# Optimization experiments

Hardware: AMD Instinct MI355X
Metric: run time of the kernel (lower is better)

Reference implementation:

```python
import jax, jax.numpy as jnp
import numpy as np

B = 2097152


def _pairwise_overlap(amin, amax, bmin, bmax):
    # amin/amax: [B,4]; bmin/bmax: [B,4] -> pairwise overlap [B,4,4]
    lo = jnp.maximum(amin[:, :, None], bmin[:, None, :])
    hi = jnptofloat = jnp.minimum(amax[:, :, None], bmax[:, None, :])
    return jnp.maximum(0.0, hi - lo)


def _self_beta(xmin, xmax, ymin, ymax):
    # sum over 4x4 pairs; diagonal terms squared, off-diagonal plain.
    xo = _pairwise_overlap(xmin, xmax, xmin, xmax)  # [B,4,4]
    yo = _pairwise_overlap(ymin, ymax, ymin, ymax)  # [B,4,4]
    area = xo * yo
    eye = jnp.eye(4, dtype=bool)
    return jnp.sum(jnp.where(eye, area * area, area), axis=(1, 2))  # [B]


def setup_inputs() -> dict:
    key = jax.random.key(0)
    k1, k2 = jax.random.split(key)
    true = jax.random.uniform(k1, (B, 4, 4), dtype=jnp.float32)
    pred = jax.random.uniform(k2, (B, 10, 3), dtype=jnp.float32)
    return {"true": true, "pred": pred}


def reference(true, pred):
    # true: [B,4,4] -> per-box coords, each [B,4]
    minx1, miny1, maxx1, maxy1 = [true[:, :, i] for i in range(4)]
    # pred: [B,10,3] -> columns [B,10]; only first 4 boxes used by the 4x4 loops
    fminx, miny2, fmaxx = pred[:, :, 0], pred[:, :, 1], pred[:, :, 2]
    minx2 = jnp.minimum(fminx, fmaxx)
    maxx2 = jnp.maximum(fminx, fmaxx)
    maxy2 = miny2 + (maxx2 - minx2)
    minx2, maxx2, miny2, maxy2 = (a[:, :4] for a in (minx2, maxx2, miny2, maxy2))

    # intersection: sum over all 4x4 (true_i, pred_j) pairs
    xo = _pairwise_overlap(minx1, maxx1, minx2, maxx2)
    yo = _pairwise_overlap(miny1, maxy1, miny2, maxy2)
    intersection = jnp.sum(xo * yo, axis=(1, 2))  # [B]

    beta1 = _self_beta(minx1, maxx1, miny1, maxy1)
    beta2 = _self_beta(minx2, maxx2, miny2, maxy2)

    loss = (beta1 - beta2) ** 2 - intersection  # [B]
    return loss[:, None]  # [B,1], matching the original's [:, i] slicing shape
```

## Files before the change

kernel.cpp:

```cpp
#include <hip/hip_runtime.h>


__global__ __launch_bounds__(256) void boxloss_kernel(
    const float* __restrict__ T, const float* __restrict__ P,
    float* __restrict__ out, int B)
{
    int b = blockIdx.x * blockDim.x + threadIdx.x;
    if (b >= B) return;

    float tmnx[4], tmny[4], tmxx[4], tmxy[4];
    const float4* T4 = reinterpret_cast<const float4*>(T) + (size_t)b * 4;
    #pragma unroll
    for (int i = 0; i < 4; ++i) {
        float4 t = T4[i];
        tmnx[i] = t.x; tmny[i] = t.y; tmxx[i] = t.z; tmxy[i] = t.w;
    }

    const float2* P2 = reinterpret_cast<const float2*>(P + (size_t)b * 30);
    float f[12];
    #pragma unroll
    for (int k = 0; k < 6; ++k) {
        float2 q = P2[k];
        f[2 * k] = q.x; f[2 * k + 1] = q.y;
    }
    float pmnx[4], pmny[4], pmxx[4], pmxy[4];
    #pragma unroll
    for (int j = 0; j < 4; ++j) {
        float p0 = f[3 * j], p1 = f[3 * j + 1], p2 = f[3 * j + 2];
        float mn = fminf(p0, p2), mx = fmaxf(p0, p2);
        pmnx[j] = mn; pmxx[j] = mx; pmny[j] = p1; pmxy[j] = p1 + (mx - mn);
    }

    float inter = 0.f, b1 = 0.f, b2 = 0.f;
    #pragma unroll
    for (int i = 0; i < 4; ++i) {
        #pragma unroll
        for (int j = 0; j < 4; ++j) {
            float xo = fmaxf(0.f, fminf(tmxx[i], pmxx[j]) - fmaxf(tmnx[i], pmnx[j]));
            float yo = fmaxf(0.f, fminf(tmxy[i], pmxy[j]) - fmaxf(tmny[i], pmny[j]));
            inter += xo * yo;
            float x1 = fmaxf(0.f, fminf(tmxx[i], tmxx[j]) - fmaxf(tmnx[i], tmnx[j]));
            float y1 = fmaxf(0.f, fminf(tmxy[i], tmxy[j]) - fmaxf(tmny[i], tmny[j]));
            float a1 = x1 * y1;
            float x2 = fmaxf(0.f, fminf(pmxx[i], pmxx[j]) - fmaxf(pmnx[i], pmnx[j]));
            float y2 = fmaxf(0.f, fminf(pmxy[i], pmxy[j]) - fmaxf(pmny[i], pmny[j]));
            float a2 = x2 * y2;
            b1 += (i == j) ? a1 * a1 : a1;
            b2 += (i == j) ? a2 * a2 : a2;
        }
    }
    float d = b1 - b2;
    out[b] = d * d - inter;
}

extern "C" void kernel_launch(void* const* d_in, const int* in_sizes, int n_in,
                              void* d_out, int out_size, void* d_ws, size_t ws_size,
                              hipStream_t stream)
{
    const float* T = (const float*)d_in[0];
    const float* P = (const float*)d_in[1];
    float* out = (float*)d_out;
    int B = in_sizes[0] / 16;

    int block = 256;
    int grid = (B + block - 1) / block;
    boxloss_kernel<<<grid, block, 0, stream>>>(T, P, out, B);
}
```

Before: 71.65 us.

## Process two records per thread with float4 loads and exploit pairwise symmetry

Each thread now handles a pair of records, so the pred rows can be read with aligned float4 loads (two records span 60 floats) and the two outputs are written as one float2. The self-overlap sums use the symmetry of the 4x4 pair matrix, computing only the upper triangle doubled plus simplified diagonal terms. This cuts both the ALU work and the number of memory instructions per record. In exchange, each thread holds more registers and the grid has half as many threads. The diagonal simplification for pred relies on its width and height being non-negative by construction.

```diff
diff --git a/kernel.cpp b/kernel.cpp
--- a/kernel.cpp
+++ b/kernel.cpp
@@ -1,37 +1,19 @@
 #include <hip/hip_runtime.h>
 
 
-__global__ __launch_bounds__(256) void boxloss_kernel(
-    const float* __restrict__ T, const float* __restrict__ P,
-    float* __restrict__ out, int B)
+__device__ __forceinline__ float record_loss(
+    const float tmnx[4], const float tmny[4], const float tmxx[4], const float tmxy[4],
+    const float pf[12])
 {
-    int b = blockIdx.x * blockDim.x + threadIdx.x;
-    if (b >= B) return;
-
-    float tmnx[4], tmny[4], tmxx[4], tmxy[4];
-    const float4* T4 = reinterpret_cast<const float4*>(T) + (size_t)b * 4;
-    #pragma unroll
-    for (int i = 0; i < 4; ++i) {
-        float4 t = T4[i];
-        tmnx[i] = t.x; tmny[i] = t.y; tmxx[i] = t.z; tmxy[i] = t.w;
-    }
-
-    const float2* P2 = reinterpret_cast<const float2*>(P + (size_t)b * 30);
-    float f[12];
-    #pragma unroll
-    for (int k = 0; k < 6; ++k) {
-        float2 q = P2[k];
-        f[2 * k] = q.x; f[2 * k + 1] = q.y;
-    }
     float pmnx[4], pmny[4], pmxx[4], pmxy[4];
     #pragma unroll
     for (int j = 0; j < 4; ++j) {
-        float p0 = f[3 * j], p1 = f[3 * j + 1], p2 = f[3 * j + 2];
+        float p0 = pf[3 * j], p1 = pf[3 * j + 1], p2 = pf[3 * j + 2];
         float mn = fminf(p0, p2), mx = fmaxf(p0, p2);
         pmnx[j] = mn; pmxx[j] = mx; pmny[j] = p1; pmxy[j] = p1 + (mx - mn);
     }
 
-    float inter = 0.f, b1 = 0.f, b2 = 0.f;
+    float inter = 0.f;
     #pragma unroll
     for (int i = 0; i < 4; ++i) {
         #pragma unroll
@@ -39,18 +21,91 @@
             float xo = fmaxf(0.f, fminf(tmxx[i], pmxx[j]) - fmaxf(tmnx[i], pmnx[j]));
             float yo = fmaxf(0.f, fminf(tmxy[i], pmxy[j]) - fmaxf(tmny[i], pmny[j]));
             inter += xo * yo;
+        }
+    }
+
+    float b1 = 0.f, b2 = 0.f;
+    #pragma unroll
+    for (int i = 0; i < 4; ++i) {
+        float w1 = fmaxf(0.f, tmxx[i] - tmnx[i]);
+        float h1 = fmaxf(0.f, tmxy[i] - tmny[i]);
+        float a1 = w1 * h1;
+        float w2 = pmxx[i] - pmnx[i];
+        float h2 = pmxy[i] - pmny[i];
+        float a2 = w2 * h2;
+        b1 += a1 * a1;
+        b2 += a2 * a2;
+    }
+    #pragma unroll
+    for (int i = 0; i < 4; ++i) {
+        #pragma unroll
+        for (int j = i + 1; j < 4; ++j) {
             float x1 = fmaxf(0.f, fminf(tmxx[i], tmxx[j]) - fmaxf(tmnx[i], tmnx[j]));
             float y1 = fmaxf(0.f, fminf(tmxy[i], tmxy[j]) - fmaxf(tmny[i], tmny[j]));
-            float a1 = x1 * y1;
+            b1 += 2.f * (x1 * y1);
             float x2 = fmaxf(0.f, fminf(pmxx[i], pmxx[j]) - fmaxf(pmnx[i], pmnx[j]));
             float y2 = fmaxf(0.f, fminf(pmxy[i], pmxy[j]) - fmaxf(pmny[i], pmny[j]));
-            float a2 = x2 * y2;
-            b1 += (i == j) ? a1 * a1 : a1;
-            b2 += (i == j) ? a2 * a2 : a2;
+            b2 += 2.f * (x2 * y2);
         }
     }
     float d = b1 - b2;
-    out[b] = d * d - inter;
+    return d * d - inter;
+}
+
+__global__ __launch_bounds__(256) void boxloss_kernel(
+    const float* __restrict__ T, const float* __restrict__ P,
+    float* __restrict__ out, int B)
+{
+    const int t = blockIdx.x * blockDim.x + threadIdx.x;
+    const int nPairs = (B + 1) >> 1;
+    if (t >= nPairs) return;
+    const bool hasB = (2 * t + 1) < B;
+
+    const float4* T4 = reinterpret_cast<const float4*>(T) + (size_t)t * 8;
+    float4 tv[8];
+    #pragma unroll
+    for (int k = 0; k < 4; ++k) tv[k] = T4[k];
+    if (hasB) {
+        #pragma unroll
+        for (int k = 4; k < 8; ++k) tv[k] = T4[k];
+    }
+
+    const float4* P4 = reinterpret_cast<const float4*>(P) + (size_t)t * 15;
+    float4 v0 = P4[0], v1 = P4[1], v2 = P4[2];
+    float4 v7, v8, v9, v10;
+    if (hasB) { v7 = P4[7]; v8 = P4[8]; v9 = P4[9]; v10 = P4[10]; }
+
+    float lossA, lossB = 0.f;
+    {
+        float tmnx[4], tmny[4], tmxx[4], tmxy[4];
+        #pragma unroll
+        for (int i = 0; i < 4; ++i) {
+            tmnx[i] = (&tv[0])[i].x; tmny[i] = (&tv[0])[i].y;
+            tmxx[i] = (&tv[0])[i].z; tmxy[i] = (&tv[0])[i].w;
+        }
+        float pf[12] = { v0.x, v0.y, v0.z, v0.w, v1.x, v1.y, v1.z, v1.w,
+                         v2.x, v2.y, v2.z, v2.w };
+        lossA = record_loss(tmnx, tmny, tmxx, tmxy, pf);
+    }
+
+    if (hasB) {
+        float tmnx[4], tmny[4], tmxx[4], tmxy[4];
+        #pragma unroll
+        for (int i = 0; i < 4; ++i) {
+            tmnx[i] = (&tv[4])[i].x; tmny[i] = (&tv[4])[i].y;
+            tmxx[i] = (&tv[4])[i].z; tmxy[i] = (&tv[4])[i].w;
+        }
+        float pf[12] = { v7.z, v7.w, v8.x, v8.y, v8.z, v8.w,
+                         v9.x, v9.y, v9.z, v9.w, v10.x, v10.y };
+        lossB = record_loss(tmnx, tmny, tmxx, tmxy, pf);
+    }
+
+    if (hasB) {
+        float2 r; r.x = lossA; r.y = lossB;
+        reinterpret_cast<float2*>(out)[t] = r;
+    } else {
+        out[2 * t] = lossA;
+    }
 }
 
 extern "C" void kernel_launch(void* const* d_in, const int* in_sizes, int n_in,
@@ -62,7 +117,8 @@
     float* out = (float*)d_out;
     int B = in_sizes[0] / 16;
 
+    int nPairs = (B + 1) / 2;
     int block = 256;
-    int grid = (B + block - 1) / block;
+    int grid = (nPairs + block - 1) / block;
     boxloss_kernel<<<grid, block, 0, stream>>>(T, P, out, B);
 }
```

After: 79.85 us. +11.4%, slower.
